# Performance work log

Measured on AMD Instinct MI355X. Metric: run time of the kernel, lower is better.

The kernel has to match this reference:

```python
import jax, jax.numpy as jnp
import numpy as np


def gcn_layer(x, src, dst, W, b, n_dst):
    # DGL GraphConv, norm='both': D_src^{-1/2} pre-norm, sum aggregate, D_dst^{-1/2} post-norm, + bias
    n_src = x.shape[0]
    e_ones = jnp.ones(src.shape[0], dtype=x.dtype)
    deg_out = jnp.clip(jax.ops.segment_sum(e_ones, src, num_segments=n_src), 1.0)
    deg_in = jnp.clip(jax.ops.segment_sum(e_ones, dst, num_segments=n_dst), 1.0)
    h = (x * jax.lax.rsqrt(deg_out)[:, None]) @ W          # [n_src, out]
    agg = jax.ops.segment_sum(h[src], dst, num_segments=n_dst)  # [n_dst, out]
    return jax.nn.relu(agg * jax.lax.rsqrt(deg_in)[:, None] + b)


def setup_inputs() -> dict:
    key = jax.random.key(0)
    ks = jax.random.split(key, 8)
    N_SRC0, N_DST0, N_DST1 = 400000, 40000, 4000
    E0, E1 = 400000, 40000
    D_IN, D_HID, D_OUT = 256, 256, 256
    x = jax.random.normal(ks[0], (N_SRC0, D_IN), dtype=jnp.float32)
    src0 = jax.random.randint(ks[1], (E0,), 0, N_SRC0)
    dst0 = jax.random.randint(ks[2], (E0,), 0, N_DST0)
    src1 = jax.random.randint(ks[3], (E1,), 0, N_DST0)
    dst1 = jax.random.randint(ks[4], (E1,), 0, N_DST1)
    W0 = jax.random.normal(ks[5], (D_IN, D_HID), dtype=jnp.float32) * (1.0 / np.sqrt(D_IN))
    W1 = jax.random.normal(ks[6], (D_HID, D_OUT), dtype=jnp.float32) * (1.0 / np.sqrt(D_HID))
    b0 = jnp.zeros((D_HID,), dtype=jnp.float32)
    b1 = jnp.zeros((D_OUT,), dtype=jnp.float32)
    return {"x": x, "src0": src0, "dst0": dst0, "src1": src1, "dst1": dst1,
            "W0": W0, "b0": b0, "W1": W1, "b1": b1,
            "n_dst0": N_DST0, "n_dst1": N_DST1}


def reference(x, src0, dst0, src1, dst1, W0, b0, W1, b1, n_dst0, n_dst1):
    h = gcn_layer(x, src0, dst0, W0, b0, n_dst0)   # [n_dst0, hidden]
    out = gcn_layer(h, src1, dst1, W1, b1, n_dst1)  # [n_dst1, out]
    return out
```

## Files before the change

### kernel.cpp

```cpp
#include <hip/hip_runtime.h>
#include <hip/hip_bf16.h>
#include <cstddef>
#include <cstdint>


#define D 256
#define N_DST0_CONST 40000
#define CAP 64
#define LDSK 264

typedef __attribute__((ext_vector_type(8))) short s16x8;
typedef __attribute__((ext_vector_type(4))) short s16x4;
typedef __attribute__((ext_vector_type(4))) float f32x4;

__device__ inline short f2bf(float f) {
    __hip_bfloat16 h = __float2bfloat16(f);
    return *reinterpret_cast<short*>(&h);
}
__device__ inline float bf2f(short s) {
    unsigned u = ((unsigned)(unsigned short)s) << 16;
    return __uint_as_float(u);
}

__global__ void zero_i(int* __restrict__ p, int n) {
    int i = blockIdx.x * blockDim.x + threadIdx.x;
    int stride = gridDim.x * blockDim.x;
    for (; i < n; i += stride) p[i] = 0;
}

__global__ __launch_bounds__(256) void build_adj_tr_both(
    const int* __restrict__ src0, const int* __restrict__ dst0, int E0,
    const int* __restrict__ src1, const int* __restrict__ dst1, int E1,
    int* __restrict__ cs0, int* __restrict__ cd0,
    int* __restrict__ cs1, int* __restrict__ cd1,
    int* __restrict__ es0, int* __restrict__ es1,
    int nEdgeBlocks,
    const float* __restrict__ Wa, short* __restrict__ BTa,
    const float* __restrict__ Wb, short* __restrict__ BTb) {
    int b = blockIdx.x;
    if (b < nEdgeBlocks) {
        int e = b * 256 + threadIdx.x;
        if (e < E0) {
            int s = src0[e], d = dst0[e];
            atomicAdd(&cs0[s], 1);
            int pos = atomicAdd(&cd0[d], 1);
            if (pos < CAP) es0[(size_t)d * CAP + pos] = s;
        } else if (e < E0 + E1) {
            int i = e - E0;
            int s = src1[i], d = dst1[i];
            atomicAdd(&cs1[s], 1);
            int pos = atomicAdd(&cd1[d], 1);
            if (pos < CAP) es1[(size_t)d * CAP + pos] = s;
        }
        return;
    }
    int t = b - nEdgeBlocks;
    const float* W = (t < 256) ? Wa : Wb;
    short* BT = (t < 256) ? BTa : BTb;
    t &= 255;
    int k0 = (t & 15) * 16;
    int n0 = (t >> 4) * 16;
    __shared__ float tile[16][17];
    int tx = threadIdx.x & 15, ty = threadIdx.x >> 4;
    tile[ty][tx] = W[(size_t)(k0 + ty) * D + n0 + tx];
    __syncthreads();
    BT[(size_t)(n0 + ty) * D + k0 + tx] = f2bf(tile[tx][ty]);
}

template<bool XF32, bool OUTF32, int MT, bool USE_MASK>
__global__ __launch_bounds__(256) void gcn_fused(
    const void* __restrict__ Xv, const int* __restrict__ edge_src,
    const int* __restrict__ cnt_src,
    const int* __restrict__ needed, const int* __restrict__ cnt_dst,
    const float* __restrict__ bias, const short* __restrict__ BT,
    void* __restrict__ outv, int nrows) {
    __shared__ short As[MT][LDSK];
    const int tid = threadIdx.x;
    const int wave = tid >> 6;
    const int lane = tid & 63;
    const int m0 = blockIdx.x * MT;
    constexpr int RPW = MT / 4;
    constexpr int NMT = MT / 16;

    const float* Xf = (const float*)Xv;
    const short* Xh = (const short*)Xv;

    for (int rr = 0; rr < RPW; ++rr) {
        int row = wave * RPW + rr;
        int d = m0 + row;
        if (d >= nrows) break;
        if (USE_MASK && needed[d] == 0) continue;
        int nb = min(cnt_dst[d], CAP);

        int s_l = 0;
        float rn_l = 0.f;
        if (lane < nb) {
            s_l = edge_src[(size_t)d * CAP + lane];
            rn_l = rsqrtf(fmaxf((float)cnt_src[s_l], 1.0f));
        }

        float4 acc = make_float4(0.f, 0.f, 0.f, 0.f);
        int j = 0;
        for (; j + 4 <= nb; j += 4) {
            int s0 = __shfl(s_l, j + 0), s1 = __shfl(s_l, j + 1);
            int s2 = __shfl(s_l, j + 2), s3 = __shfl(s_l, j + 3);
            float r0 = __shfl(rn_l, j + 0), r1 = __shfl(rn_l, j + 1);
            float r2 = __shfl(rn_l, j + 2), r3 = __shfl(rn_l, j + 3);
            float4 v0, v1, v2, v3;
            if (XF32) {
                v0 = *(const float4*)(Xf + (size_t)s0 * D + lane * 4);
                v1 = *(const float4*)(Xf + (size_t)s1 * D + lane * 4);
                v2 = *(const float4*)(Xf + (size_t)s2 * D + lane * 4);
                v3 = *(const float4*)(Xf + (size_t)s3 * D + lane * 4);
            } else {
                s16x4 a = *(const s16x4*)(Xh + (size_t)s0 * D + lane * 4);
                s16x4 b = *(const s16x4*)(Xh + (size_t)s1 * D + lane * 4);
                s16x4 c = *(const s16x4*)(Xh + (size_t)s2 * D + lane * 4);
                s16x4 e = *(const s16x4*)(Xh + (size_t)s3 * D + lane * 4);
                v0 = make_float4(bf2f(a.x), bf2f(a.y), bf2f(a.z), bf2f(a.w));
                v1 = make_float4(bf2f(b.x), bf2f(b.y), bf2f(b.z), bf2f(b.w));
                v2 = make_float4(bf2f(c.x), bf2f(c.y), bf2f(c.z), bf2f(c.w));
                v3 = make_float4(bf2f(e.x), bf2f(e.y), bf2f(e.z), bf2f(e.w));
            }
            acc.x += v0.x * r0 + v1.x * r1 + v2.x * r2 + v3.x * r3;
            acc.y += v0.y * r0 + v1.y * r1 + v2.y * r2 + v3.y * r3;
            acc.z += v0.z * r0 + v1.z * r1 + v2.z * r2 + v3.z * r3;
            acc.w += v0.w * r0 + v1.w * r1 + v2.w * r2 + v3.w * r3;
        }
        for (; j < nb; ++j) {
            int s = __shfl(s_l, j);
            float r = __shfl(rn_l, j);
            float4 v;
            if (XF32) {
                v = *(const float4*)(Xf + (size_t)s * D + lane * 4);
            } else {
                s16x4 a = *(const s16x4*)(Xh + (size_t)s * D + lane * 4);
                v = make_float4(bf2f(a.x), bf2f(a.y), bf2f(a.z), bf2f(a.w));
            }
            acc.x += v.x * r; acc.y += v.y * r; acc.z += v.z * r; acc.w += v.w * r;
        }

        s16x4 o;
        o.x = f2bf(acc.x); o.y = f2bf(acc.y); o.z = f2bf(acc.z); o.w = f2bf(acc.w);
        *(s16x4*)&As[row][lane * 4] = o;
    }
    __syncthreads();

    const int l15 = lane & 15;
    const int quad = lane >> 4;
    const int n0w = wave * 64;

    f32x4 acc[NMT][4] = {};
    for (int k0 = 0; k0 < D; k0 += 32) {
        s16x8 af[NMT], bfr[4];
#pragma unroll
        for (int nt = 0; nt < 4; ++nt)
            bfr[nt] = *(const s16x8*)(BT + (size_t)(n0w + nt * 16 + l15) * D + k0 + quad * 8);
#pragma unroll
        for (int mt = 0; mt < NMT; ++mt)
            af[mt] = *(const s16x8*)&As[mt * 16 + l15][k0 + quad * 8];
#pragma unroll
        for (int mt = 0; mt < NMT; ++mt)
#pragma unroll
            for (int nt = 0; nt < 4; ++nt)
                acc[mt][nt] = __builtin_amdgcn_mfma_f32_16x16x32_bf16(
                    af[mt], bfr[nt], acc[mt][nt], 0, 0, 0);
    }

#pragma unroll
    for (int mt = 0; mt < NMT; ++mt) {
#pragma unroll
        for (int r = 0; r < 4; ++r) {
            int gm = m0 + mt * 16 + quad * 4 + r;
            if (gm >= nrows) continue;
            if (USE_MASK && needed[gm] == 0) continue;
            float sc = rsqrtf(fmaxf((float)cnt_dst[gm], 1.0f));
#pragma unroll
            for (int nt = 0; nt < 4; ++nt) {
                int gn = n0w + nt * 16 + l15;
                float v = fmaxf(acc[mt][nt][r] * sc + bias[gn], 0.f);
                if (OUTF32) ((float*)outv)[(size_t)gm * D + gn] = v;
                else        ((short*)outv)[(size_t)gm * D + gn] = f2bf(v);
            }
        }
    }
}


extern "C" void kernel_launch(void* const* d_in, const int* in_sizes, int n_in,
                              void* d_out, int out_size, void* d_ws, size_t ws_size,
                              hipStream_t stream) {
    const float* x    = (const float*)d_in[0];
    const int*   src0 = (const int*)d_in[1];
    const int*   dst0 = (const int*)d_in[2];
    const int*   src1 = (const int*)d_in[3];
    const int*   dst1 = (const int*)d_in[4];
    const float* W0   = (const float*)d_in[5];
    const float* b0   = (const float*)d_in[6];
    const float* W1   = (const float*)d_in[7];
    const float* b1   = (const float*)d_in[8];

    const int n_src0 = in_sizes[0] / D;
    const int E0     = in_sizes[1];
    const int E1     = in_sizes[3];
    const int n_dst0 = N_DST0_CONST;
    const int n_dst1 = out_size / D;

    char* base = (char*)d_ws;
    size_t off = 0;
    auto alloc = [&](size_t bytes) { void* p = base + off; off = (off + bytes + 63) & ~(size_t)63; return p; };

    int* icnt = (int*)alloc((size_t)(n_src0 + 2 * n_dst0 + n_dst1) * 4);
    int* icnt_src0 = icnt;
    int* icnt_dst0 = icnt + n_src0;
    int* icnt_src1 = icnt + n_src0 + n_dst0;
    int* icnt_dst1 = icnt + n_src0 + 2 * n_dst0;
    const int cnt_total = n_src0 + 2 * n_dst0 + n_dst1;

    int* es0 = (int*)alloc((size_t)n_dst0 * CAP * 4);
    int* es1 = (int*)alloc((size_t)n_dst1 * CAP * 4);

    short* h0b = (short*)alloc((size_t)n_dst0 * D * 2);
    short* BT0 = (short*)alloc((size_t)D * D * 2);
    short* BT1 = (short*)alloc((size_t)D * D * 2);

    float* out = (float*)d_out;

    zero_i<<<512, 256, 0, stream>>>(icnt, cnt_total);

    const int nEdgeBlocks = (E0 + E1 + 255) / 256;
    build_adj_tr_both<<<nEdgeBlocks + 512, 256, 0, stream>>>(
        src0, dst0, E0, src1, dst1, E1,
        icnt_src0, icnt_dst0, icnt_src1, icnt_dst1,
        es0, es1, nEdgeBlocks, W0, BT0, W1, BT1);

    gcn_fused<true, false, 64, true><<<(n_dst0 + 63) / 64, 256, 0, stream>>>(
        x, es0, icnt_src0, icnt_src1, icnt_dst0, b0, BT0, h0b, n_dst0);

    gcn_fused<false, true, 16, false><<<(n_dst1 + 15) / 16, 256, 0, stream>>>(
        h0b, es1, icnt_src1, nullptr, icnt_dst1, b1, BT1, out, n_dst1);
}
```

Baseline: 602.4 us.

## Compact live layer-0 rows into a list and unroll gather by eight

```diff
diff --git a/kernel.cpp b/kernel.cpp
--- a/kernel.cpp
+++ b/kernel.cpp
@@ -34,6 +34,7 @@
     int* __restrict__ cs0, int* __restrict__ cd0,
     int* __restrict__ cs1, int* __restrict__ cd1,
     int* __restrict__ es0, int* __restrict__ es1,
+    int* __restrict__ live, int* __restrict__ nlive,
     int nEdgeBlocks,
     const float* __restrict__ Wa, short* __restrict__ BTa,
     const float* __restrict__ Wb, short* __restrict__ BTb) {
@@ -48,7 +49,8 @@
         } else if (e < E0 + E1) {
             int i = e - E0;
             int s = src1[i], d = dst1[i];
-            atomicAdd(&cs1[s], 1);
+            int p = atomicAdd(&cs1[s], 1);
+            if (p == 0) { int idx = atomicAdd(nlive, 1); live[idx] = s; }
             int pos = atomicAdd(&cd1[d], 1);
             if (pos < CAP) es1[(size_t)d * CAP + pos] = s;
         }
@@ -67,14 +69,16 @@
     BT[(size_t)(n0 + ty) * D + k0 + tx] = f2bf(tile[tx][ty]);
 }
 
-template<bool XF32, bool OUTF32, int MT, bool USE_MASK>
+template<bool XF32, bool OUTF32, int MT, bool COMPACT>
 __global__ __launch_bounds__(256) void gcn_fused(
     const void* __restrict__ Xv, const int* __restrict__ edge_src,
     const int* __restrict__ cnt_src,
-    const int* __restrict__ needed, const int* __restrict__ cnt_dst,
+    const int* __restrict__ live, const int* __restrict__ nlive_p,
+    const int* __restrict__ cnt_dst,
     const float* __restrict__ bias, const short* __restrict__ BT,
     void* __restrict__ outv, int nrows) {
     __shared__ short As[MT][LDSK];
+    __shared__ int lidx[MT];
     const int tid = threadIdx.x;
     const int wave = tid >> 6;
     const int lane = tid & 63;
@@ -82,14 +86,18 @@
     constexpr int RPW = MT / 4;
     constexpr int NMT = MT / 16;
 
+    const int nl = COMPACT ? *nlive_p : nrows;
+    if (m0 >= nl) return;
+
     const float* Xf = (const float*)Xv;
     const short* Xh = (const short*)Xv;
 
     for (int rr = 0; rr < RPW; ++rr) {
         int row = wave * RPW + rr;
-        int d = m0 + row;
-        if (d >= nrows) break;
-        if (USE_MASK && needed[d] == 0) continue;
+        int g = m0 + row;
+        int d = (g < nl) ? (COMPACT ? live[g] : g) : -1;
+        if (lane == 0) lidx[row] = d;
+        if (d < 0) continue;
         int nb = min(cnt_dst[d], CAP);
 
         int s_l = 0;
@@ -98,46 +106,35 @@
             s_l = edge_src[(size_t)d * CAP + lane];
             rn_l = rsqrtf(fmaxf((float)cnt_src[s_l], 1.0f));
         }
+        int slast = __shfl(s_l, (nb > 0) ? nb - 1 : 0);
+        if (lane >= nb) { s_l = slast; rn_l = 0.f; }
+        int nbr = (nb + 7) & ~7;
 
         float4 acc = make_float4(0.f, 0.f, 0.f, 0.f);
-        int j = 0;
-        for (; j + 4 <= nb; j += 4) {
-            int s0 = __shfl(s_l, j + 0), s1 = __shfl(s_l, j + 1);
-            int s2 = __shfl(s_l, j + 2), s3 = __shfl(s_l, j + 3);
-            float r0 = __shfl(rn_l, j + 0), r1 = __shfl(rn_l, j + 1);
-            float r2 = __shfl(rn_l, j + 2), r3 = __shfl(rn_l, j + 3);
-            float4 v0, v1, v2, v3;
-            if (XF32) {
-                v0 = *(const float4*)(Xf + (size_t)s0 * D + lane * 4);
-                v1 = *(const float4*)(Xf + (size_t)s1 * D + lane * 4);
-                v2 = *(const float4*)(Xf + (size_t)s2 * D + lane * 4);
-                v3 = *(const float4*)(Xf + (size_t)s3 * D + lane * 4);
-            } else {
-                s16x4 a = *(const s16x4*)(Xh + (size_t)s0 * D + lane * 4);
-                s16x4 b = *(const s16x4*)(Xh + (size_t)s1 * D + lane * 4);
-                s16x4 c = *(const s16x4*)(Xh + (size_t)s2 * D + lane * 4);
-                s16x4 e = *(const s16x4*)(Xh + (size_t)s3 * D + lane * 4);
-                v0 = make_float4(bf2f(a.x), bf2f(a.y), bf2f(a.z), bf2f(a.w));
-                v1 = make_float4(bf2f(b.x), bf2f(b.y), bf2f(b.z), bf2f(b.w));
-                v2 = make_float4(bf2f(c.x), bf2f(c.y), bf2f(c.z), bf2f(c.w));
-                v3 = make_float4(bf2f(e.x), bf2f(e.y), bf2f(e.z), bf2f(e.w));
-            }
-            acc.x += v0.x * r0 + v1.x * r1 + v2.x * r2 + v3.x * r3;
-            acc.y += v0.y * r0 + v1.y * r1 + v2.y * r2 + v3.y * r3;
-            acc.z += v0.z * r0 + v1.z * r1 + v2.z * r2 + v3.z * r3;
-            acc.w += v0.w * r0 + v1.w * r1 + v2.w * r2 + v3.w * r3;
-        }
-        for (; j < nb; ++j) {
-            int s = __shfl(s_l, j);
-            float r = __shfl(rn_l, j);
-            float4 v;
-            if (XF32) {
-                v = *(const float4*)(Xf + (size_t)s * D + lane * 4);
-            } else {
-                s16x4 a = *(const s16x4*)(Xh + (size_t)s * D + lane * 4);
-                v = make_float4(bf2f(a.x), bf2f(a.y), bf2f(a.z), bf2f(a.w));
-            }
-            acc.x += v.x * r; acc.y += v.y * r; acc.z += v.z * r; acc.w += v.w * r;
+        for (int j = 0; j < nbr; j += 8) {
+            int si[8]; float ri[8];
+#pragma unroll
+            for (int u = 0; u < 8; ++u) {
+                si[u] = __shfl(s_l, j + u);
+                ri[u] = __shfl(rn_l, j + u);
+            }
+            float4 v[8];
+#pragma unroll
+            for (int u = 0; u < 8; ++u) {
+                if (XF32) {
+                    v[u] = *(const float4*)(Xf + (size_t)si[u] * D + lane * 4);
+                } else {
+                    s16x4 a = *(const s16x4*)(Xh + (size_t)si[u] * D + lane * 4);
+                    v[u] = make_float4(bf2f(a.x), bf2f(a.y), bf2f(a.z), bf2f(a.w));
+                }
+            }
+#pragma unroll
+            for (int u = 0; u < 8; ++u) {
+                acc.x += v[u].x * ri[u];
+                acc.y += v[u].y * ri[u];
+                acc.z += v[u].z * ri[u];
+                acc.w += v[u].w * ri[u];
+            }
         }
 
         s16x4 o;
@@ -171,9 +168,9 @@
     for (int mt = 0; mt < NMT; ++mt) {
 #pragma unroll
         for (int r = 0; r < 4; ++r) {
-            int gm = m0 + mt * 16 + quad * 4 + r;
-            if (gm >= nrows) continue;
-            if (USE_MASK && needed[gm] == 0) continue;
+            int row = mt * 16 + quad * 4 + r;
+            int gm = lidx[row];
+            if (gm < 0) continue;
             float sc = rsqrtf(fmaxf((float)cnt_dst[gm], 1.0f));
 #pragma unroll
             for (int nt = 0; nt < 4; ++nt) {
@@ -210,15 +207,17 @@
     size_t off = 0;
     auto alloc = [&](size_t bytes) { void* p = base + off; off = (off + bytes + 63) & ~(size_t)63; return p; };
 
-    int* icnt = (int*)alloc((size_t)(n_src0 + 2 * n_dst0 + n_dst1) * 4);
+    int* icnt = (int*)alloc((size_t)(n_src0 + 2 * n_dst0 + n_dst1 + 64) * 4);
     int* icnt_src0 = icnt;
     int* icnt_dst0 = icnt + n_src0;
     int* icnt_src1 = icnt + n_src0 + n_dst0;
     int* icnt_dst1 = icnt + n_src0 + 2 * n_dst0;
-    const int cnt_total = n_src0 + 2 * n_dst0 + n_dst1;
-
-    int* es0 = (int*)alloc((size_t)n_dst0 * CAP * 4);
-    int* es1 = (int*)alloc((size_t)n_dst1 * CAP * 4);
+    int* nlive     = icnt + n_src0 + 2 * n_dst0 + n_dst1;
+    const int cnt_total = n_src0 + 2 * n_dst0 + n_dst1 + 1;
+
+    int* es0  = (int*)alloc((size_t)n_dst0 * CAP * 4);
+    int* es1  = (int*)alloc((size_t)n_dst1 * CAP * 4);
+    int* live = (int*)alloc((size_t)n_dst0 * 4);
 
     short* h0b = (short*)alloc((size_t)n_dst0 * D * 2);
     short* BT0 = (short*)alloc((size_t)D * D * 2);
@@ -232,11 +231,11 @@
     build_adj_tr_both<<<nEdgeBlocks + 512, 256, 0, stream>>>(
         src0, dst0, E0, src1, dst1, E1,
         icnt_src0, icnt_dst0, icnt_src1, icnt_dst1,
-        es0, es1, nEdgeBlocks, W0, BT0, W1, BT1);
+        es0, es1, live, nlive, nEdgeBlocks, W0, BT0, W1, BT1);
 
     gcn_fused<true, false, 64, true><<<(n_dst0 + 63) / 64, 256, 0, stream>>>(
-        x, es0, icnt_src0, icnt_src1, icnt_dst0, b0, BT0, h0b, n_dst0);
+        x, es0, icnt_src0, live, nlive, icnt_dst0, b0, BT0, h0b, n_dst0);
 
     gcn_fused<false, true, 16, false><<<(n_dst1 + 15) / 16, 256, 0, stream>>>(
-        h0b, es1, icnt_src1, nullptr, icnt_dst1, b1, BT1, out, n_dst1);
-}
+        h0b, es1, icnt_src1, nullptr, nullptr, icnt_dst1, b1, BT1, out, n_dst1);
+}
```

New measurement: 592.8 us. No clear change (-1.6%).
